# Kernel tuning notes

Hardware: AMD Instinct MI355X
Metric: run time of the kernel (lower is better)

## Reference

```python
import jax, jax.numpy as jnp
import numpy as np

V = 10000      # char vocab / out_size
EMB = 512      # char embedding dim
H = 1024       # GRU hidden size
NL = 2         # GRU layers
SEQ = 64       # encoder char sequence length
MAXLEN = 64    # decode steps
OUT = V


def _gru_cell(x, h, Wih, Whh, bih, bhh):
    # PyTorch GRU cell, gate order (r, z, n)
    gi = x @ Wih.T + bih
    gh = h @ Whh.T + bhh
    ir, iz, inn = jnp.split(gi, 3, axis=-1)
    hr, hz, hn = jnp.split(gh, 3, axis=-1)
    r = jax.nn.sigmoid(ir + hr)
    z = jax.nn.sigmoid(iz + hz)
    n = jnp.tanh(inn + r * hn)
    return (1.0 - z) * n + z * h


def _run_gru(layers, h0, xs):
    # layers: list of (Wih, Whh, bih, bhh); h0: (NL, H); xs: (T, in)
    def step(h, x):
        hs = []
        inp = x
        for l, p in enumerate(layers):
            hn = _gru_cell(inp, h[l], *p)
            hs.append(hn)
            inp = hn
        return jnp.stack(hs), inp
    return jax.lax.scan(step, h0, xs)


def setup_inputs():
    key = jax.random.key(0)
    ks = list(jax.random.split(key, 32))
    def nrm(k, shape, s=0.02):
        return jax.random.normal(k, shape, jnp.float32) * s
    d = {}
    # ids in [2, V): pad id 0 and eos id 1 never occur -> mask all-True, no early break
    d["char_seq"] = jax.random.randint(ks[0], (SEQ,), 2, V, dtype=jnp.int32)
    d["enc_state"] = nrm(ks[1], (NL * H,), 0.1)
    d["sos"] = jnp.array([2], dtype=jnp.int32)
    d["eos"] = 1
    d["max_len"] = MAXLEN
    d["target_char_seq"] = jax.random.randint(ks[2], (MAXLEN,), 2, V, dtype=jnp.int32)
    d["emb_table"] = nrm(ks[3], (V, EMB))
    i = 4
    for pre in ("enc", "dec"):
        for l in range(NL):
            ind = EMB if l == 0 else H
            d[f"{pre}_Wih{l}"] = nrm(ks[i], (3 * H, ind)); i += 1
            d[f"{pre}_Whh{l}"] = nrm(ks[i], (3 * H, H)); i += 1
            d[f"{pre}_bih{l}"] = jnp.zeros((3 * H,), jnp.float32)
            d[f"{pre}_bhh{l}"] = jnp.zeros((3 * H,), jnp.float32)
    d["out_W"] = nrm(ks[i], (OUT, H)); i += 1
    d["out_b"] = jnp.zeros((OUT,), jnp.float32)
    return d


def reference(char_seq, enc_state, sos, eos, max_len, target_char_seq, emb_table,
              enc_Wih0, enc_Whh0, enc_bih0, enc_bhh0, enc_Wih1, enc_Whh1, enc_bih1, enc_bhh1,
              dec_Wih0, dec_Whh0, dec_bih0, dec_bhh0, dec_Wih1, dec_Whh1, dec_bih1, dec_bhh1,
              out_W, out_b):
    enc_layers = [(enc_Wih0, enc_Whh0, enc_bih0, enc_bhh0),
                  (enc_Wih1, enc_Whh1, enc_bih1, enc_bhh1)]
    dec_layers = [(dec_Wih0, dec_Whh0, dec_bih0, dec_bhh0),
                  (dec_Wih1, dec_Whh1, dec_bih1, dec_bhh1)]
    # mask = char_seq != 0 is all-True by construction (ids >= 2), so gather everything
    emb_chars = emb_table[char_seq]                  # (SEQ, EMB)
    # torch: view(1,1,-1), split into NL chunks along feat, cat on layer dim == reshape
    h0 = enc_state.reshape(NL, H)
    dec_h0, _ = _run_gru(enc_layers, h0, emb_chars)  # final hidden -> decoder init
    # teacher forcing: step t consumes sos then target[t-1]; eos never hit -> full max_len
    dec_in = jnp.concatenate([sos, target_char_seq[: max_len - 1]])
    emb_dec = emb_table[dec_in]                      # (max_len, EMB)

    def dec_step(h, x):
        hs = []
        inp = x
        for l, p in enumerate(dec_layers):
            hn = _gru_cell(inp, h[l], *p)
            hs.append(hn)
            inp = hn
        h_new = jnp.stack(hs)
        scores = inp @ out_W.T + out_b               # out_dropout identity (eval)
        return h_new, (scores, h_new.reshape(-1))

    _, (dec_scores, dec_states) = jax.lax.scan(dec_step, dec_h0, emb_dec)
    # fill_len == 0 (no early eos break), F.pad is a no-op
    return dec_scores[None, :, :], dec_states[None, :, :]
```

## Files before the change

### kernel.cpp

```cpp
#include <hip/hip_runtime.h>
#include <hip/hip_bf16.h>
#include <math.h>

#define V     10000
#define EMB   512
#define H     1024
#define H3    3072
#define SEQ   64
#define NPAD  10048
#define NPH   129

typedef __attribute__((ext_vector_type(8))) unsigned short us8;
typedef __attribute__((ext_vector_type(8))) unsigned u32x8;
typedef unsigned long long ull;

__device__ __forceinline__ float sigmoidf_(float x) { return 1.0f / (1.0f + expf(-x)); }
__device__ __forceinline__ float bf2f(unsigned short u) { return __uint_as_float(((unsigned)u) << 16); }
__device__ __forceinline__ float lof(unsigned u) { return __uint_as_float(u << 16); }
__device__ __forceinline__ float hif(unsigned u) { return __uint_as_float(u & 0xffff0000u); }
__device__ __forceinline__ unsigned short f2bf_rne(float f) {
    unsigned u = __float_as_uint(f);
    unsigned r = u + 0x7FFF + ((u >> 16) & 1);
    return (unsigned short)(r >> 16);
}
__device__ __forceinline__ ull packh(float v) {
    return (ull)__float_as_uint(v) | (1ULL << 32);
}

struct CvtArgs { const float* src[6]; unsigned short* dst0; };
__global__ __launch_bounds__(256) void f2bf6_kernel(CvtArgs c) {
    const float* src = c.src[blockIdx.y];
    unsigned short* dst = c.dst0 + (size_t)blockIdx.y * ((size_t)H3 * H);
    int i = (blockIdx.x * 256 + threadIdx.x) * 8;
    float4 a = *(const float4*)(src + i);
    float4 b = *(const float4*)(src + i + 4);
    us8 o;
    o[0] = f2bf_rne(a.x); o[1] = f2bf_rne(a.y); o[2] = f2bf_rne(a.z); o[3] = f2bf_rne(a.w);
    o[4] = f2bf_rne(b.x); o[5] = f2bf_rne(b.y); o[6] = f2bf_rne(b.z); o[7] = f2bf_rne(b.w);
    *(us8*)(dst + i) = o;
}

__global__ __launch_bounds__(256) void init2_kernel(const float* __restrict__ enc_state,
                                                    ull* __restrict__ h0hist, ull* __restrict__ h1hist,
                                                    float* __restrict__ h0buf, float* __restrict__ h1buf) {
    int i = blockIdx.x * 256 + threadIdx.x;
    if (i >= NPH * 1024) return;
    ull v0 = 0, v1 = 0;
    if (i < 1024) {
        v0 = packh(enc_state[i]);
        v1 = packh(enc_state[H + i]);
        h0buf[i] = enc_state[i];
        h1buf[H + i] = enc_state[H + i];
    }
    h0hist[i] = v0;
    h1hist[i] = v1;
}

__global__ void embed_kernel(const int* __restrict__ cs, const int* __restrict__ sos,
                             const int* __restrict__ tgt, const float* __restrict__ emb,
                             float* __restrict__ e_enc, float* __restrict__ e_dec) {
    int t = blockIdx.x;
    int id;
    float* dst;
    if (t < SEQ) { id = cs[t]; dst = e_enc + (size_t)t * EMB; }
    else         { int td = t - SEQ; id = (td == 0) ? sos[0] : tgt[td - 1]; dst = e_dec + (size_t)td * EMB; }
    const float4* src4 = (const float4*)(emb + (size_t)id * EMB);
    float4* dst4 = (float4*)dst;
    dst4[threadIdx.x] = src4[threadIdx.x];
}

__global__ __launch_bounds__(256) void gi_gemm_kernel(const float* __restrict__ Ae, const float* __restrict__ We,
                                                      const float* __restrict__ be, float* __restrict__ oe,
                                                      const float* __restrict__ Ad, const float* __restrict__ Wd,
                                                      const float* __restrict__ bd, float* __restrict__ od) {
    __shared__ float As[64][64 + 1];
    __shared__ float Bs[64][64 + 1];
    const float* A = blockIdx.y ? Ad : Ae;
    const float* W = blockIdx.y ? Wd : We;
    const float* bias = blockIdx.y ? bd : be;
    float* out = blockIdx.y ? od : oe;
    int n0 = blockIdx.x * 64;
    int tid = threadIdx.x;
    int tn = tid & 15, tm = tid >> 4;
    float acc[4][4] = {};
    for (int k0 = 0; k0 < EMB; k0 += 64) {
        for (int i = tid; i < 64 * 16; i += 256) {
            int m = i >> 4, kq = i & 15;
            float4 v = *(const float4*)(A + (size_t)m * EMB + k0 + kq * 4);
            As[kq * 4 + 0][m] = v.x; As[kq * 4 + 1][m] = v.y;
            As[kq * 4 + 2][m] = v.z; As[kq * 4 + 3][m] = v.w;
        }
        for (int i = tid; i < 64 * 16; i += 256) {
            int n = i >> 4, kq = i & 15;
            float4 v = *(const float4*)(W + (size_t)(n0 + n) * EMB + k0 + kq * 4);
            Bs[kq * 4 + 0][n] = v.x; Bs[kq * 4 + 1][n] = v.y;
            Bs[kq * 4 + 2][n] = v.z; Bs[kq * 4 + 3][n] = v.w;
        }
        __syncthreads();
        #pragma unroll 8
        for (int k = 0; k < 64; ++k) {
            float a[4], b[4];
            #pragma unroll
            for (int i = 0; i < 4; ++i) a[i] = As[k][tm * 4 + i];
            #pragma unroll
            for (int j = 0; j < 4; ++j) b[j] = Bs[k][tn * 4 + j];
            #pragma unroll
            for (int i = 0; i < 4; ++i)
                #pragma unroll
                for (int j = 0; j < 4; ++j) acc[i][j] += a[i] * b[j];
        }
        __syncthreads();
    }
    #pragma unroll
    for (int i = 0; i < 4; ++i) {
        int m = tm * 4 + i;
        #pragma unroll
        for (int j = 0; j < 4; ++j) {
            int r = n0 + tn * 4 + j;
            out[(size_t)m * H3 + r] = acc[i][j] + bias[r];
        }
    }
}

struct PArgs {
    const unsigned short *encWhh0, *encWih1, *encWhh1;
    const unsigned short *decWhh0, *decWih1, *decWhh1;
    const float *gi_enc0, *gi_dec0;
    const float *enc_bhh0, *dec_bhh0;
    const float *enc_bih1, *enc_bhh1, *dec_bih1, *dec_bhh1;
    ull *h0hist, *h1hist;
    float *states;
};

__device__ __forceinline__ void loadw24(const unsigned short* __restrict__ m,
                                        int j, int lane,
                                        u32x8& w0, u32x8& w1, u32x8& w2) {
    size_t b0 = (size_t)j * H + lane;
    size_t b1 = (size_t)(H + j) * H + lane;
    size_t b2 = (size_t)(2 * H + j) * H + lane;
    #pragma unroll
    for (int q = 0; q < 8; ++q) {
        w0[q] = (unsigned)m[b0 + 128 * q] | ((unsigned)m[b0 + 128 * q + 64] << 16);
        w1[q] = (unsigned)m[b1 + 128 * q] | ((unsigned)m[b1 + 128 * q + 64] << 16);
        w2[q] = (unsigned)m[b2 + 128 * q] | ((unsigned)m[b2 + 128 * q + 64] << 16);
    }
}

__global__ __launch_bounds__(1024, 4) void persist_kernel(PArgs a) {
    __shared__ __align__(16) float xh0[H];
    __shared__ __align__(16) float xh1[H];
    __shared__ float sred[64];
    const int tid = threadIdx.x;
    const int w = tid >> 6, lane = tid & 63;
    const int bid = blockIdx.x;

    if (bid < 64) {
        const int j = bid * 16 + w;
        u32x8 w0, w1, w2;
        loadw24(a.encWhh0, j, lane, w0, w1, w2);
        float b0 = 0.f, b1 = 0.f, b2 = 0.f, g0 = 0.f, g1 = 0.f, g2 = 0.f;
        if (lane == 0) {
            b0 = a.enc_bhh0[j]; b1 = a.enc_bhh0[H + j]; b2 = a.enc_bhh0[2 * H + j];
            g0 = a.gi_enc0[j];  g1 = a.gi_enc0[H + j];  g2 = a.gi_enc0[2 * H + j];
        }
        for (int p = 0; p < 128; ++p) {
            {
                const ull* src = a.h0hist + (size_t)p * 1024 + tid;
                ull v = __hip_atomic_load(src, __ATOMIC_RELAXED, __HIP_MEMORY_SCOPE_AGENT);
                while (!(v >> 32)) {
                    __builtin_amdgcn_s_sleep(1);
                    v = __hip_atomic_load(src, __ATOMIC_RELAXED, __HIP_MEMORY_SCOPE_AGENT);
                }
                xh0[tid] = __uint_as_float((unsigned)v);
            }
            __syncthreads();
            float s0 = 0.f, s1 = 0.f, s2 = 0.f;
            #pragma unroll
            for (int q = 0; q < 8; ++q) {
                float x0 = xh0[lane + 128 * q];
                float x1 = xh0[lane + 128 * q + 64];
                s0 += lof(w0[q]) * x0 + hif(w0[q]) * x1;
                s1 += lof(w1[q]) * x0 + hif(w1[q]) * x1;
                s2 += lof(w2[q]) * x0 + hif(w2[q]) * x1;
            }
            #pragma unroll
            for (int m = 1; m < 64; m <<= 1) {
                s0 += __shfl_xor(s0, m);
                s1 += __shfl_xor(s1, m);
                s2 += __shfl_xor(s2, m);
            }
            if (lane == 0) {
                float r = sigmoidf_(g0 + s0 + b0);
                float z = sigmoidf_(g1 + s1 + b1);
                float n = tanhf(g2 + r * (s2 + b2));
                float hn = (1.f - z) * n + z * xh0[j];
                __hip_atomic_store(a.h0hist + (size_t)(p + 1) * 1024 + j, packh(hn),
                                   __ATOMIC_RELAXED, __HIP_MEMORY_SCOPE_AGENT);
                if (p >= 64) a.states[(size_t)(p - 64) * 2048 + j] = hn;
                if (p < 127) {
                    const float* gn = (p + 1 < 64) ? (a.gi_enc0 + (size_t)(p + 1) * H3)
                                                   : (a.gi_dec0 + (size_t)(p + 1 - 64) * H3);
                    g0 = gn[j]; g1 = gn[H + j]; g2 = gn[2 * H + j];
                }
            }
            if (p == 63) {
                loadw24(a.decWhh0, j, lane, w0, w1, w2);
                if (lane == 0) { b0 = a.dec_bhh0[j]; b1 = a.dec_bhh0[H + j]; b2 = a.dec_bhh0[2 * H + j]; }
            }
            __syncthreads();
        }
    } else {
        const int bb = bid - 64;
        const int j = bb * 8 + (w >> 1);
        const int part = w & 1;
        u32x8 w0, w1, w2;
        loadw24(part == 0 ? a.encWih1 : a.encWhh1, j, lane, w0, w1, w2);
        float b0 = 0.f, b1 = 0.f, b2 = 0.f, b3 = 0.f, b4 = 0.f, b5 = 0.f;
        if (tid < 8) {
            int jg = bb * 8 + tid;
            b0 = a.enc_bih1[jg]; b1 = a.enc_bih1[H + jg]; b2 = a.enc_bih1[2 * H + jg];
            b3 = a.enc_bhh1[jg]; b4 = a.enc_bhh1[H + jg]; b5 = a.enc_bhh1[2 * H + jg];
        }
        for (int p = 1; p <= 128; ++p) {
            {
                const ull* s0p = a.h0hist + (size_t)p * 1024 + tid;
                const ull* s1p = a.h1hist + (size_t)(p - 1) * 1024 + tid;
                ull v0 = __hip_atomic_load(s0p, __ATOMIC_RELAXED, __HIP_MEMORY_SCOPE_AGENT);
                ull v1 = __hip_atomic_load(s1p, __ATOMIC_RELAXED, __HIP_MEMORY_SCOPE_AGENT);
                while (!(v0 >> 32) || !(v1 >> 32)) {
                    __builtin_amdgcn_s_sleep(1);
                    if (!(v0 >> 32)) v0 = __hip_atomic_load(s0p, __ATOMIC_RELAXED, __HIP_MEMORY_SCOPE_AGENT);
                    if (!(v1 >> 32)) v1 = __hip_atomic_load(s1p, __ATOMIC_RELAXED, __HIP_MEMORY_SCOPE_AGENT);
                }
                xh0[tid] = __uint_as_float((unsigned)v0);
                xh1[tid] = __uint_as_float((unsigned)v1);
            }
            __syncthreads();
            {
                const float* x = (part == 0) ? xh0 : xh1;
                float s0 = 0.f, s1 = 0.f, s2 = 0.f;
                #pragma unroll
                for (int q = 0; q < 8; ++q) {
                    float x0 = x[lane + 128 * q];
                    float x1 = x[lane + 128 * q + 64];
                    s0 += lof(w0[q]) * x0 + hif(w0[q]) * x1;
                    s1 += lof(w1[q]) * x0 + hif(w1[q]) * x1;
                    s2 += lof(w2[q]) * x0 + hif(w2[q]) * x1;
                }
                #pragma unroll
                for (int m = 1; m < 64; m <<= 1) {
                    s0 += __shfl_xor(s0, m);
                    s1 += __shfl_xor(s1, m);
                    s2 += __shfl_xor(s2, m);
                }
                if (lane == 0) {
                    int slot = (w >> 1) * 8 + part * 4;
                    sred[slot + 0] = s0; sred[slot + 1] = s1; sred[slot + 2] = s2;
                }
            }
            __syncthreads();
            if (tid < 8) {
                int jg = bb * 8 + tid;
                float si0 = sred[tid * 8 + 0], si1 = sred[tid * 8 + 1], si2 = sred[tid * 8 + 2];
                float sh0 = sred[tid * 8 + 4], sh1 = sred[tid * 8 + 5], sh2 = sred[tid * 8 + 6];
                float r = sigmoidf_(si0 + b0 + sh0 + b3);
                float z = sigmoidf_(si1 + b1 + sh1 + b4);
                float n = tanhf(si2 + b2 + r * (sh2 + b5));
                float hn = (1.f - z) * n + z * xh1[jg];
                __hip_atomic_store(a.h1hist + (size_t)p * 1024 + jg, packh(hn),
                                   __ATOMIC_RELAXED, __HIP_MEMORY_SCOPE_AGENT);
                if (p >= 65) a.states[(size_t)(p - 65) * 2048 + H + jg] = hn;
            }
            if (p == 64) {
                loadw24(part == 0 ? a.decWih1 : a.decWhh1, j, lane, w0, w1, w2);
                if (tid < 8) {
                    int jg = bb * 8 + tid;
                    b0 = a.dec_bih1[jg]; b1 = a.dec_bih1[H + jg]; b2 = a.dec_bih1[2 * H + jg];
                    b3 = a.dec_bhh1[jg]; b4 = a.dec_bhh1[H + jg]; b5 = a.dec_bhh1[2 * H + jg];
                }
            }
            __syncthreads();
        }
    }
}

template<int BF>
__global__ __launch_bounds__(384) void phase_kernel(
    const float* __restrict__ giA, const void* __restrict__ WhhA, const float* __restrict__ bhhA,
    const float* __restrict__ h0r, float* __restrict__ h0w, float* __restrict__ statesA, int hasA,
    const void* __restrict__ WihB, const float* __restrict__ bihB,
    const void* __restrict__ WhhB, const float* __restrict__ bhhB,
    const float* __restrict__ h1r, float* __restrict__ h1w, float* __restrict__ statesB, int hasB) {
    __shared__ float sred[8];
    int bid = blockIdx.x;
    int tid = threadIdx.x;
    int w = tid >> 6, lane = tid & 63;
    auto dotf = [&](const void* Wp, size_t roff, const float* x) -> float {
        float s = 0.f;
        if (BF) {
            const unsigned short* wrow = (const unsigned short*)Wp + roff;
            #pragma unroll
            for (int i = 0; i < 2; ++i) {
                int k = lane * 8 + i * 512;
                us8 wv = *(const us8*)(wrow + k);
                float4 x0 = *(const float4*)(x + k);
                float4 x1 = *(const float4*)(x + k + 4);
                s += bf2f(wv[0]) * x0.x + bf2f(wv[1]) * x0.y + bf2f(wv[2]) * x0.z + bf2f(wv[3]) * x0.w
                   + bf2f(wv[4]) * x1.x + bf2f(wv[5]) * x1.y + bf2f(wv[6]) * x1.z + bf2f(wv[7]) * x1.w;
            }
        } else {
            const float* wrow = (const float*)Wp + roff;
            #pragma unroll
            for (int i = 0; i < 4; ++i) {
                int k = lane * 4 + i * 256;
                float4 wv = *(const float4*)(wrow + k);
                float4 xv = *(const float4*)(x + k);
                s += wv.x * xv.x + wv.y * xv.y + wv.z * xv.z + wv.w * xv.w;
            }
        }
        return s;
    };
    if (bid < 512) {
        if (!hasA) return;
        int tt = w / 3, g = w - tt * 3;
        int jj = bid * 2 + tt;
        float s = dotf(WhhA, (size_t)(g * H + jj) * H, h0r);
        #pragma unroll
        for (int m = 1; m < 64; m <<= 1) s += __shfl_xor(s, m);
        if (lane == 0) sred[w] = s;
        __syncthreads();
        if (tid < 2) {
            int j2 = bid * 2 + tid;
            float s0 = sred[tid * 3], s1 = sred[tid * 3 + 1], s2 = sred[tid * 3 + 2];
            float r = sigmoidf_(giA[j2] + s0 + bhhA[j2]);
            float z = sigmoidf_(giA[H + j2] + s1 + bhhA[H + j2]);
            float n = tanhf(giA[2 * H + j2] + r * (s2 + bhhA[2 * H + j2]));
            float hn = (1.f - z) * n + z * h0r[j2];
            h0w[j2] = hn;
            if (statesA) statesA[j2] = hn;
        }
    } else {
        if (!hasB) return;
        int j = bid - 512;
        int hh = (w >= 3);
        int g = w - hh * 3;
        float s = dotf(hh ? WhhB : WihB, (size_t)(g * H + j) * H, hh ? h1r : h0r);
        #pragma unroll
        for (int m = 1; m < 64; m <<= 1) s += __shfl_xor(s, m);
        if (lane == 0) sred[w] = s;
        __syncthreads();
        if (tid == 0) {
            float r = sigmoidf_(sred[0] + bihB[j] + sred[3] + bhhB[j]);
            float z = sigmoidf_(sred[1] + bihB[H + j] + sred[4] + bhhB[H + j]);
            float n = tanhf(sred[2] + bihB[2 * H + j] + r * (sred[5] + bhhB[2 * H + j]));
            float hn = (1.f - z) * n + z * h1r[j];
            h1w[j] = hn;
            if (statesB) statesB[j] = hn;
        }
    }
}

#define SN 64
#define SK 64
__global__ __launch_bounds__(256) void scores_kernel(const float* __restrict__ states,
                                                     const float* __restrict__ W,
                                                     const float* __restrict__ bias,
                                                     float* __restrict__ dst, int kc_count) {
    __shared__ float As[SK][64 + 1];
    __shared__ float Bs[SK][SN + 1];
    int n0 = blockIdx.x * SN;
    int kc = blockIdx.y;
    int klen = H / kc_count;
    int kbeg = kc * klen;
    int tid = threadIdx.x;
    int tn = tid & 15, tm = tid >> 4;
    float acc[4][4] = {};
    for (int k0 = kbeg; k0 < kbeg + klen; k0 += SK) {
        for (int i = tid; i < 64 * (SK / 4); i += 256) {
            int m = i >> 4;
            int kq = i & 15;
            float4 v = *(const float4*)(states + (size_t)m * 2048 + H + k0 + kq * 4);
            As[kq * 4 + 0][m] = v.x; As[kq * 4 + 1][m] = v.y;
            As[kq * 4 + 2][m] = v.z; As[kq * 4 + 3][m] = v.w;
        }
        for (int i = tid; i < SN * (SK / 4); i += 256) {
            int n = i >> 4;
            int kq = i & 15;
            int r = n0 + n;
            float4 v = make_float4(0.f, 0.f, 0.f, 0.f);
            if (r < V) v = *(const float4*)(W + (size_t)r * H + k0 + kq * 4);
            Bs[kq * 4 + 0][n] = v.x; Bs[kq * 4 + 1][n] = v.y;
            Bs[kq * 4 + 2][n] = v.z; Bs[kq * 4 + 3][n] = v.w;
        }
        __syncthreads();
        #pragma unroll 8
        for (int k = 0; k < SK; ++k) {
            float a[4], b[4];
            #pragma unroll
            for (int i = 0; i < 4; ++i) a[i] = As[k][tm * 4 + i];
            #pragma unroll
            for (int j = 0; j < 4; ++j) b[j] = Bs[k][tn * 4 + j];
            #pragma unroll
            for (int i = 0; i < 4; ++i)
                #pragma unroll
                for (int j = 0; j < 4; ++j) acc[i][j] += a[i] * b[j];
        }
        __syncthreads();
    }
    if (kc_count == 1) {
        #pragma unroll
        for (int i = 0; i < 4; ++i) {
            int m = tm * 4 + i;
            #pragma unroll
            for (int j = 0; j < 4; ++j) {
                int r = n0 + tn * 4 + j;
                if (r < V) dst[(size_t)m * V + r] = acc[i][j] + bias[r];
            }
        }
    } else {
        #pragma unroll
        for (int i = 0; i < 4; ++i) {
            int m = tm * 4 + i;
            #pragma unroll
            for (int j = 0; j < 4; ++j) {
                int r = n0 + tn * 4 + j;
                dst[(size_t)(kc * 64 + m) * NPAD + r] = acc[i][j];
            }
        }
    }
}

__global__ __launch_bounds__(256) void reduce_scores_kernel(const float* __restrict__ part,
                                                            const float* __restrict__ bias,
                                                            float* __restrict__ out, int kc_count) {
    int e = blockIdx.x * 256 + threadIdx.x;
    if (e >= 64 * V) return;
    int m = e / V, r = e - m * V;
    float s = bias[r];
    for (int kc = 0; kc < kc_count; ++kc)
        s += part[(size_t)(kc * 64 + m) * NPAD + r];
    out[(size_t)m * V + r] = s;
}

extern "C" void kernel_launch(void* const* d_in, const int* in_sizes, int n_in,
                              void* d_out, int out_size, void* d_ws, size_t ws_size,
                              hipStream_t stream) {
    const int*   char_seq  = (const int*)d_in[0];
    const float* enc_state = (const float*)d_in[1];
    const int*   sos       = (const int*)d_in[2];
    const int*   tgt       = (const int*)d_in[5];
    const float* emb       = (const float*)d_in[6];
    const float* enc_Wih0  = (const float*)d_in[7];
    const float* enc_Whh0  = (const float*)d_in[8];
    const float* enc_bih0  = (const float*)d_in[9];
    const float* enc_bhh0  = (const float*)d_in[10];
    const float* enc_Wih1  = (const float*)d_in[11];
    const float* enc_Whh1  = (const float*)d_in[12];
    const float* enc_bih1  = (const float*)d_in[13];
    const float* enc_bhh1  = (const float*)d_in[14];
    const float* dec_Wih0  = (const float*)d_in[15];
    const float* dec_Whh0  = (const float*)d_in[16];
    const float* dec_bih0  = (const float*)d_in[17];
    const float* dec_bhh0  = (const float*)d_in[18];
    const float* dec_Wih1  = (const float*)d_in[19];
    const float* dec_Whh1  = (const float*)d_in[20];
    const float* dec_bih1  = (const float*)d_in[21];
    const float* dec_bhh1  = (const float*)d_in[22];
    const float* out_W     = (const float*)d_in[23];
    const float* out_b     = (const float*)d_in[24];

    float* ws = (float*)d_ws;
    float* e_enc   = ws;
    float* e_dec   = e_enc + SEQ * EMB;
    float* gi_enc0 = e_dec + SEQ * EMB;
    float* gi_dec0 = gi_enc0 + SEQ * H3;
    ull*   h0hist  = (ull*)(gi_dec0 + SEQ * H3);
    ull*   h1hist  = h0hist + (size_t)NPH * 1024;
    float* h0buf   = (float*)(h1hist + (size_t)NPH * 1024);
    float* h1buf   = h0buf + 2 * H;
    float* cur     = h1buf + 2 * H;
    size_t base = (size_t)(cur - ws);
    size_t avail = ws_size / 4 > base ? ws_size / 4 - base : 0;

    const size_t REC_ELEMS = (size_t)H3 * H;
    const size_t REC_SLOTS = REC_ELEMS / 2;

    int bf_rec = (avail >= 6 * REC_SLOTS);
    unsigned short* wbf0 = nullptr;
    if (bf_rec) { wbf0 = (unsigned short*)cur; cur += 6 * REC_SLOTS; avail -= 6 * REC_SLOTS; }
    int KC = 1;
    if (avail >= (size_t)8 * 64 * NPAD) KC = 8;
    else if (avail >= (size_t)4 * 64 * NPAD) KC = 4;
    else if (avail >= (size_t)2 * 64 * NPAD) KC = 2;
    float* partials = cur;

    float* scores = (float*)d_out;
    float* states = scores + SEQ * V;

    if (bf_rec) {
        CvtArgs c;
        c.src[0] = enc_Whh0; c.src[1] = enc_Wih1; c.src[2] = enc_Whh1;
        c.src[3] = dec_Whh0; c.src[4] = dec_Wih1; c.src[5] = dec_Whh1;
        c.dst0 = wbf0;
        f2bf6_kernel<<<dim3((unsigned)(REC_ELEMS / 2048), 6), 256, 0, stream>>>(c);
    }
    init2_kernel<<<(NPH * 1024 + 255) / 256, 256, 0, stream>>>(enc_state, h0hist, h1hist, h0buf, h1buf);
    embed_kernel<<<128, 128, 0, stream>>>(char_seq, sos, tgt, emb, e_enc, e_dec);
    gi_gemm_kernel<<<dim3(H3 / 64, 2), 256, 0, stream>>>(e_enc, enc_Wih0, enc_bih0, gi_enc0,
                                                         e_dec, dec_Wih0, dec_bih0, gi_dec0);

    bool done = false;
    if (bf_rec) {
        PArgs pa;
        pa.encWhh0 = wbf0;
        pa.encWih1 = wbf0 + REC_ELEMS;
        pa.encWhh1 = wbf0 + 2 * REC_ELEMS;
        pa.decWhh0 = wbf0 + 3 * REC_ELEMS;
        pa.decWih1 = wbf0 + 4 * REC_ELEMS;
        pa.decWhh1 = wbf0 + 5 * REC_ELEMS;
        pa.gi_enc0 = gi_enc0; pa.gi_dec0 = gi_dec0;
        pa.enc_bhh0 = enc_bhh0; pa.dec_bhh0 = dec_bhh0;
        pa.enc_bih1 = enc_bih1; pa.enc_bhh1 = enc_bhh1;
        pa.dec_bih1 = dec_bih1; pa.dec_bhh1 = dec_bhh1;
        pa.h0hist = h0hist; pa.h1hist = h1hist; pa.states = states;
        void* kparams[] = { (void*)&pa };
        hipError_t err = hipLaunchCooperativeKernel((const void*)persist_kernel,
                                                    dim3(192), dim3(1024), kparams, 0, stream);
        done = (err == hipSuccess);
    }

    if (!done) {
        for (int p = 0; p <= 128; ++p) {
            int hasA = (p <= 127);
            int hasB = (p >= 1);
            const float* giA = nullptr; const void* WhhA = nullptr; const float* bhhA = nullptr;
            float* statesA = nullptr;
            if (hasA) {
                if (p < 64) {
                    giA = gi_enc0 + (size_t)p * H3; bhhA = enc_bhh0;
                    WhhA = bf_rec ? (const void*)wbf0 : (const void*)enc_Whh0;
                } else {
                    int t = p - 64;
                    giA = gi_dec0 + (size_t)t * H3; bhhA = dec_bhh0;
                    WhhA = bf_rec ? (const void*)(wbf0 + 3 * REC_ELEMS) : (const void*)dec_Whh0;
                    statesA = states + (size_t)t * 2048;
                }
            }
            const void *WihB = nullptr, *WhhB = nullptr;
            const float *bihB = nullptr, *bhhB = nullptr;
            float* statesB = nullptr;
            if (hasB) {
                if (p <= 64) {
                    bihB = enc_bih1; bhhB = enc_bhh1;
                    WihB = bf_rec ? (const void*)(wbf0 + REC_ELEMS) : (const void*)enc_Wih1;
                    WhhB = bf_rec ? (const void*)(wbf0 + 2 * REC_ELEMS) : (const void*)enc_Whh1;
                } else {
                    int t = p - 65;
                    bihB = dec_bih1; bhhB = dec_bhh1;
                    WihB = bf_rec ? (const void*)(wbf0 + 4 * REC_ELEMS) : (const void*)dec_Wih1;
                    WhhB = bf_rec ? (const void*)(wbf0 + 5 * REC_ELEMS) : (const void*)dec_Whh1;
                    statesB = states + (size_t)t * 2048 + H;
                }
            }
            float* h0r = h0buf + (p & 1) * H;
            float* h0w = h0buf + ((p + 1) & 1) * H;
            float* h1r = h1buf + (p & 1) * H;
            float* h1w = h1buf + ((p + 1) & 1) * H;
            if (bf_rec)
                phase_kernel<1><<<1536, 384, 0, stream>>>(giA, WhhA, bhhA, h0r, h0w, statesA, hasA,
                                                          WihB, bihB, WhhB, bhhB, h1r, h1w, statesB, hasB);
            else
                phase_kernel<0><<<1536, 384, 0, stream>>>(giA, WhhA, bhhA, h0r, h0w, statesA, hasA,
                                                          WihB, bihB, WhhB, bhhB, h1r, h1w, statesB, hasB);
        }
    }

    if (KC == 1) {
        scores_kernel<<<dim3((V + SN - 1) / SN, 1), 256, 0, stream>>>(states, out_W, out_b, scores, 1);
    } else {
        scores_kernel<<<dim3((V + SN - 1) / SN, KC), 256, 0, stream>>>(states, out_W, out_b, partials, KC);
        reduce_scores_kernel<<<(64 * V + 255) / 256, 256, 0, stream>>>(partials, out_b, scores, KC);
    }
}
```

Baseline: 535.9 us.

## Fuse output projection into persistent kernel, overlapping it with decoder recurrence

Adds 64 extra blocks to the cooperative persistent kernel. Each one waits for batches of 16 decoder layer-1 hidden states and computes the output-layer scores for its slice of 157 vocab rows, so the projection overlaps the serial recurrence instead of running in a separate kernel afterward. Shared memory grows to 16K floats per block to hold the batch of hidden states. This risks lower occupancy, or a failed cooperative launch with 256 blocks, and fp32 weight reads that are reloaded for each of the 4 batches.

Result: slower. 1.428 ms (+166.4%).

```diff
diff --git a/kernel.cpp b/kernel.cpp
--- a/kernel.cpp
+++ b/kernel.cpp
@@ -128,8 +128,9 @@
     const float *gi_enc0, *gi_dec0;
     const float *enc_bhh0, *dec_bhh0;
     const float *enc_bih1, *enc_bhh1, *dec_bih1, *dec_bhh1;
+    const float *outW, *outb;
     ull *h0hist, *h1hist;
-    float *states;
+    float *states, *scores;
 };
 
 __device__ __forceinline__ void loadw24(const unsigned short* __restrict__ m,
@@ -147,9 +148,10 @@
 }
 
 __global__ __launch_bounds__(1024, 4) void persist_kernel(PArgs a) {
-    __shared__ __align__(16) float xh0[H];
-    __shared__ __align__(16) float xh1[H];
-    __shared__ float sred[64];
+    __shared__ __align__(16) float pool[16 * 1024 + 64];
+    float* xh0 = pool;
+    float* xh1 = pool + 1024;
+    float* sred = pool + 2048;
     const int tid = threadIdx.x;
     const int w = tid >> 6, lane = tid & 63;
     const int bid = blockIdx.x;
@@ -209,7 +211,7 @@
             }
             __syncthreads();
         }
-    } else {
+    } else if (bid < 192) {
         const int bb = bid - 64;
         const int j = bb * 8 + (w >> 1);
         const int part = w & 1;
@@ -277,6 +279,57 @@
                     int jg = bb * 8 + tid;
                     b0 = a.dec_bih1[jg]; b1 = a.dec_bih1[H + jg]; b2 = a.dec_bih1[2 * H + jg];
                     b3 = a.dec_bhh1[jg]; b4 = a.dec_bhh1[H + jg]; b5 = a.dec_bhh1[2 * H + jg];
+                }
+            }
+            __syncthreads();
+        }
+    } else {
+        const int c = bid - 192;
+        const int r0 = c * 157;
+        const int rN = (r0 + 157 < V) ? r0 + 157 : V;
+        float* hb = pool;
+        for (int batch = 0; batch < 4; ++batch) {
+            const int pBase = 65 + batch * 16;
+            if (tid == 0) {
+                const ull* gp = a.h1hist + (size_t)(pBase + 15) * 1024 + 512;
+                while (!(__hip_atomic_load(gp, __ATOMIC_RELAXED, __HIP_MEMORY_SCOPE_AGENT) >> 32))
+                    __builtin_amdgcn_s_sleep(32);
+            }
+            __syncthreads();
+            for (int t = 0; t < 16; ++t) {
+                const ull* sp = a.h1hist + (size_t)(pBase + t) * 1024 + tid;
+                ull v = __hip_atomic_load(sp, __ATOMIC_RELAXED, __HIP_MEMORY_SCOPE_AGENT);
+                while (!(v >> 32)) {
+                    __builtin_amdgcn_s_sleep(1);
+                    v = __hip_atomic_load(sp, __ATOMIC_RELAXED, __HIP_MEMORY_SCOPE_AGENT);
+                }
+                hb[t * 1024 + tid] = __uint_as_float((unsigned)v);
+            }
+            __syncthreads();
+            for (int r = r0 + w; r < rN; r += 16) {
+                const float* wr = a.outW + (size_t)r * H;
+                float wv[16];
+                #pragma unroll
+                for (int i = 0; i < 16; ++i) wv[i] = wr[lane + 64 * i];
+                float acc[16];
+                #pragma unroll
+                for (int t = 0; t < 16; ++t) {
+                    const float* hbt = hb + t * 1024;
+                    float s = 0.f;
+                    #pragma unroll
+                    for (int i = 0; i < 16; ++i) s += wv[i] * hbt[lane + 64 * i];
+                    acc[t] = s;
+                }
+                #pragma unroll
+                for (int t = 0; t < 16; ++t) {
+                    #pragma unroll
+                    for (int m = 1; m < 64; m <<= 1) acc[t] += __shfl_xor(acc[t], m);
+                }
+                if (lane == 0) {
+                    float bb = a.outb[r];
+                    #pragma unroll
+                    for (int t = 0; t < 16; ++t)
+                        a.scores[(size_t)(batch * 16 + t) * V + r] = acc[t] + bb;
                 }
             }
             __syncthreads();
@@ -522,10 +575,12 @@
         pa.enc_bhh0 = enc_bhh0; pa.dec_bhh0 = dec_bhh0;
         pa.enc_bih1 = enc_bih1; pa.enc_bhh1 = enc_bhh1;
         pa.dec_bih1 = dec_bih1; pa.dec_bhh1 = dec_bhh1;
-        pa.h0hist = h0hist; pa.h1hist = h1hist; pa.states = states;
+        pa.outW = out_W; pa.outb = out_b;
+        pa.h0hist = h0hist; pa.h1hist = h1hist;
+        pa.states = states; pa.scores = scores;
         void* kparams[] = { (void*)&pa };
         hipError_t err = hipLaunchCooperativeKernel((const void*)persist_kernel,
-                                                    dim3(192), dim3(1024), kparams, 0, stream);
+                                                    dim3(256), dim3(1024), kparams, 0, stream);
         done = (err == hipSuccess);
     }
 
@@ -573,12 +628,11 @@
                 phase_kernel<0><<<1536, 384, 0, stream>>>(giA, WhhA, bhhA, h0r, h0w, statesA, hasA,
                                                           WihB, bihB, WhhB, bhhB, h1r, h1w, statesB, hasB);
         }
-    }
-
-    if (KC == 1) {
-        scores_kernel<<<dim3((V + SN - 1) / SN, 1), 256, 0, stream>>>(states, out_W, out_b, scores, 1);
-    } else {
-        scores_kernel<<<dim3((V + SN - 1) / SN, KC), 256, 0, stream>>>(states, out_W, out_b, partials, KC);
-        reduce_scores_kernel<<<(64 * V + 255) / 256, 256, 0, stream>>>(partials, out_b, scores, KC);
-    }
-}
+        if (KC == 1) {
+            scores_kernel<<<dim3((V + SN - 1) / SN, 1), 256, 0, stream>>>(states, out_W, out_b, scores, 1);
+        } else {
+            scores_kernel<<<dim3((V + SN - 1) / SN, KC), 256, 0, stream>>>(states, out_W, out_b, partials, KC);
+            reduce_scores_kernel<<<(64 * V + 255) / 256, 256, 0, stream>>>(partials, out_b, scores, KC);
+        }
+    }
+}
```
